# Kernel optimization log

Hardware: AMD Instinct MI355X
Metric: run time of the kernel (lower is better)

Reference implementation:

```python
import jax, jax.numpy as jnp
import numpy as np

N_NODES = 50000
N_EDGES = 800000
HID = 128
EDGE_DIM = 4
LAYERS = 4
MAX_Z = 100
NUM_GRAPHS = 512


def setup_inputs() -> dict:
    key = jax.random.key(0)
    ks = jax.random.split(key, 16)
    s = lambda k, shape, fan_in: jax.random.normal(k, shape, jnp.float32) / np.sqrt(fan_in)
    inp = {
        "z": jax.random.randint(ks[0], (N_NODES,), 0, MAX_Z + 1),
        "edge_index": jax.random.randint(ks[1], (2, N_EDGES), 0, N_NODES),
        "edge_attr": jax.random.normal(ks[2], (N_EDGES, EDGE_DIM), jnp.float32),
        "batch": jnp.sort(jax.random.randint(ks[3], (N_NODES,), 0, NUM_GRAPHS)),
        "emb": jax.random.normal(ks[4], (MAX_Z + 1, HID), jnp.float32),
        # stacked per-layer params; Linear stored as [in, out]
        "ew1": s(ks[5], (LAYERS, 2 * HID + EDGE_DIM, HID), 2 * HID + EDGE_DIM),
        "eb1": jnp.zeros((LAYERS, HID), jnp.float32),
        "ew2": s(ks[6], (LAYERS, HID, HID), HID),
        "eb2": jnp.zeros((LAYERS, HID), jnp.float32),
        "nw": s(ks[7], (LAYERS, 2 * HID, HID), 2 * HID),
        "nb": jnp.zeros((LAYERS, HID), jnp.float32),
        "rw1": s(ks[8], (HID, HID), HID),
        "rb1": jnp.zeros((HID,), jnp.float32),
        "rw2": s(ks[9], (HID, 1), HID),
        "rb2": jnp.zeros((1,), jnp.float32),
    }
    return inp


def _forward(z, edge_index, edge_attr, batch,
             emb, ew1, eb1, ew2, eb2, nw, nb, rw1, rb1, rw2, rb2):
    silu = jax.nn.silu
    src, dst = edge_index[0], edge_index[1]
    x = emb[z]  # [N, H]
    for l in range(LAYERS):
        m_in = jnp.concatenate([x[src], x[dst], edge_attr], axis=-1)  # [E, 2H+ed]
        h = silu(m_in @ ew1[l] + eb1[l])
        msg = silu(h @ ew2[l] + eb2[l])  # [E, H]
        agg = jax.ops.segment_sum(msg, dst, num_segments=N_NODES)  # scatter-add
        x = silu(jnp.concatenate([x, agg], axis=-1) @ nw[l] + nb[l])
    # segment mean over graphs
    sums = jax.ops.segment_sum(x, batch, num_segments=NUM_GRAPHS)
    counts = jnp.clip(jax.ops.segment_sum(jnp.ones((x.shape[0],), x.dtype), batch,
                                          num_segments=NUM_GRAPHS), 1.0)[:, None]
    g = sums / counts  # [G, H]
    pred = (silu(g @ rw1 + rb1) @ rw2 + rb2)[:, 0]  # [G]
    return pred


def reference(z, edge_index, edge_attr, batch,
              emb, ew1, eb1, ew2, eb2, nw, nb, rw1, rb1, rw2, rb2):
    return _forward(z, edge_index, edge_attr, batch,
                    emb, ew1, eb1, ew2, eb2, nw, nb, rw1, rb1, rw2, rb2)
```

## Files before the change

kernel.cpp:

```cpp
#include <hip/hip_runtime.h>
#include <hip/hip_bf16.h>
#include <math.h>

#define HID  128
#define EDIM 4

typedef unsigned short u16;
typedef u16    us8   __attribute__((ext_vector_type(8)));
typedef __bf16 bf16x8 __attribute__((ext_vector_type(8)));
typedef float  f32x4 __attribute__((ext_vector_type(4)));

__device__ __forceinline__ float silu_f(float v) {
    return v * __builtin_amdgcn_rcpf(1.0f + __expf(-v));
}
__device__ __forceinline__ u16 f2bf(float f) {
    unsigned u = __float_as_uint(f);
    unsigned r = u + 0x7fffu + ((u >> 16) & 1u);
    return (u16)(r >> 16);
}
__device__ __forceinline__ u16 f2bf_fast(float f) {
    return (u16)((__float_as_uint(f) + 0x8000u) >> 16);
}
__device__ __forceinline__ unsigned pack_bf2(float a, float b) {
    return ((__float_as_uint(a) + 0x8000u) >> 16) |
           ((__float_as_uint(b) + 0x8000u) & 0xffff0000u);
}
__device__ __forceinline__ float bf2f(u16 s) {
    return __uint_as_float(((unsigned)s) << 16);
}
__device__ __forceinline__ bf16x8 as_bf(us8 v) {
    return __builtin_bit_cast(bf16x8, v);
}
__device__ __forceinline__ f32x4 bf4f(ushort4 v) {
    f32x4 r;
    r[0] = bf2f(v.x); r[1] = bf2f(v.y); r[2] = bf2f(v.z); r[3] = bf2f(v.w);
    return r;
}

__device__ __forceinline__ void wfrag_gen(const float* __restrict__ w,
        u16* __restrict__ out, int KT, int Kdata, int Kstride,
        int split, int jump, int idx) {
    int lane = idx & 63;
    int f    = (idx >> 6) % (KT * 8);
    int l    = idx / (64 * KT * 8);
    int kt = f >> 3, nt = f & 7;
    int n  = nt * 16 + (lane & 15);
    int k0 = kt * 32 + ((lane >> 4) * 8);
    us8 v;
    #pragma unroll
    for (int j = 0; j < 8; ++j) {
        int k = k0 + j;
        int row = k + (k >= split ? jump : 0);
        v[j] = (row < Kdata) ? f2bf(w[((size_t)l * Kstride + row) * HID + n]) : (u16)0;
    }
    *(us8*)&out[((size_t)(l * KT * 8 + f) * 64 + lane) * 8] = v;
}

#define T1S (4 * 4 * 8 * 64)
#define T1T (4 * 1 * 8 * 64)
#define T1B (4 * 4 * 8 * 64)
#define T2  (4 * 4 * 8 * 64)
#define T3  (4 * 8 * 8 * 64)

__global__ __launch_bounds__(256) void setup_kernel(
        const float* __restrict__ ew1, const float* __restrict__ ew2,
        const float* __restrict__ nw,
        u16* __restrict__ w1sf, u16* __restrict__ w1tf,
        u16* __restrict__ w1bf,
        u16* __restrict__ w2f, u16* __restrict__ nwf,
        int* __restrict__ cnt, int* __restrict__ cursor,
        float* __restrict__ sums, float* __restrict__ cnts_g, int N, int G) {
    const int BIG = 1 << 30;
    int idx = blockIdx.x * 256 + threadIdx.x;
    if (idx < T1S) { wfrag_gen(ew1, w1sf, 4, 128, 260, BIG, 0, idx); return; }
    idx -= T1S;
    if (idx < T1T) { wfrag_gen(ew1, w1tf, 1, 260, 260, 0, 256, idx); return; }
    idx -= T1T;
    if (idx < T1B) { wfrag_gen(ew1, w1bf, 4, 260, 260, 0, 128, idx); return; }
    idx -= T1B;
    if (idx < T2) { wfrag_gen(ew2, w2f, 4, 128, 128, BIG, 0, idx); return; }
    idx -= T2;
    if (idx < T3) { wfrag_gen(nw, nwf, 8, 256, 256, BIG, 0, idx); return; }
    idx -= T3;
    if (idx < N) { cnt[idx] = 0; return; }
    idx -= N;
    if (idx < N) { cursor[idx] = 0; return; }
    idx -= N;
    if (idx < G * HID) { sums[idx] = 0.f; return; }
    idx -= G * HID;
    if (idx < G) { cnts_g[idx] = 0.f; return; }
}

__global__ __launch_bounds__(256) void hist_kernel(const int* __restrict__ dst,
        int* __restrict__ cnt, int E) {
    int e = blockIdx.x * 256 + threadIdx.x;
    if (e < E) atomicAdd(&cnt[dst[e]], 1);
}

__global__ __launch_bounds__(1024) void scan_kernel(const int* __restrict__ cnt,
        int* __restrict__ rowptr, int n) {
    __shared__ int s[1024];
    const int t = threadIdx.x;
    const int chunk = (n + 1023) >> 10;
    int lo = t * chunk, hi = lo + chunk;
    if (lo > n) lo = n;
    if (hi > n) hi = n;
    int sum = 0;
    for (int i = lo; i < hi; ++i) sum += cnt[i];
    s[t] = sum;
    __syncthreads();
    for (int off = 1; off < 1024; off <<= 1) {
        int v = (t >= off) ? s[t - off] : 0;
        __syncthreads();
        s[t] += v;
        __syncthreads();
    }
    int run = s[t] - sum;
    for (int i = lo; i < hi; ++i) { rowptr[i] = run; run += cnt[i]; }
    if (t == 1023) rowptr[n] = run;
}

__device__ __forceinline__ void dual_proj(
        const u16* __restrict__ xb,
        const u16* __restrict__ w1sf, const u16* __restrict__ w1bf,
        const float* __restrict__ b1n,
        u16* __restrict__ Ys, u16* __restrict__ Y,
        int i0, int n, int t) {
    const int wv   = t >> 6, lane = t & 63;
    const int lrow = lane & 15;
    const int kq   = lane >> 4;
    const int kq8  = kq * 8;

    int iN[2];
    #pragma unroll
    for (int mt = 0; mt < 2; ++mt) {
        int i = i0 + mt * 16 + lrow; if (i >= n) i = n - 1;
        iN[mt] = i;
    }
    f32x4 aS[2][2], aB[2][2];
    #pragma unroll
    for (int mt = 0; mt < 2; ++mt)
        #pragma unroll
        for (int nt = 0; nt < 2; ++nt) {
            aS[mt][nt] = (f32x4){0.f, 0.f, 0.f, 0.f};
            aB[mt][nt] = *(const f32x4*)&b1n[(wv * 2 + nt) * 16 + kq * 4];
        }

    #pragma unroll
    for (int kt = 0; kt < 4; ++kt) {
        bf16x8 ws0 = *(const bf16x8*)&w1sf[((size_t)(kt * 8 + wv * 2 + 0) * 64 + lane) * 8];
        bf16x8 ws1 = *(const bf16x8*)&w1sf[((size_t)(kt * 8 + wv * 2 + 1) * 64 + lane) * 8];
        bf16x8 wb0 = *(const bf16x8*)&w1bf[((size_t)(kt * 8 + wv * 2 + 0) * 64 + lane) * 8];
        bf16x8 wb1 = *(const bf16x8*)&w1bf[((size_t)(kt * 8 + wv * 2 + 1) * 64 + lane) * 8];
        #pragma unroll
        for (int mt = 0; mt < 2; ++mt) {
            bf16x8 a = as_bf(*(const us8*)&xb[(size_t)iN[mt] * HID + kt * 32 + kq8]);
            aS[mt][0] = __builtin_amdgcn_mfma_f32_16x16x32_bf16(ws0, a, aS[mt][0], 0, 0, 0);
            aS[mt][1] = __builtin_amdgcn_mfma_f32_16x16x32_bf16(ws1, a, aS[mt][1], 0, 0, 0);
            aB[mt][0] = __builtin_amdgcn_mfma_f32_16x16x32_bf16(wb0, a, aB[mt][0], 0, 0, 0);
            aB[mt][1] = __builtin_amdgcn_mfma_f32_16x16x32_bf16(wb1, a, aB[mt][1], 0, 0, 0);
        }
    }
    #pragma unroll
    for (int mt = 0; mt < 2; ++mt) {
        int node = i0 + mt * 16 + lrow;
        if (node < n) {
            #pragma unroll
            for (int nt = 0; nt < 2; ++nt) {
                uint2 sv, bv;
                sv.x = pack_bf2(aS[mt][nt][0], aS[mt][nt][1]);
                sv.y = pack_bf2(aS[mt][nt][2], aS[mt][nt][3]);
                bv.x = pack_bf2(aB[mt][nt][0], aB[mt][nt][1]);
                bv.y = pack_bf2(aB[mt][nt][2], aB[mt][nt][3]);
                *(uint2*)&Ys[(size_t)node * HID + (wv * 2 + nt) * 16 + kq * 4] = sv;
                *(uint2*)&Y [(size_t)node * HID + (wv * 2 + nt) * 16 + kq * 4] = bv;
            }
        }
    }
}

__global__ __launch_bounds__(256) void scatter_embed_kernel(
        const int* __restrict__ src, const int* __restrict__ dst,
        const float* __restrict__ ea, const int* __restrict__ rowptr,
        int* __restrict__ cursor, int4* __restrict__ es,
        const int* __restrict__ z, const float* __restrict__ emb,
        u16* __restrict__ xb, u16* __restrict__ agg,
        const int* __restrict__ batch, float* __restrict__ counts,
        const u16* __restrict__ w1sf, const u16* __restrict__ w1bf,
        const float* __restrict__ b1n,
        u16* __restrict__ Ys, u16* __restrict__ Y,
        int E, int n, int SB) {
    const int t = threadIdx.x;
    if ((int)blockIdx.x < SB) {
        int e = blockIdx.x * 256 + t;
        if (e >= E) return;
        int d = dst[e];
        int p = rowptr[d] + atomicAdd(&cursor[d], 1);
        const float* q = &ea[(size_t)e * EDIM];
        int4 rec;
        rec.x = src[e];
        rec.y = d;
        rec.z = (int)((unsigned)f2bf(q[0]) | ((unsigned)f2bf(q[1]) << 16));
        rec.w = (int)((unsigned)f2bf(q[2]) | ((unsigned)f2bf(q[3]) << 16));
        es[p] = rec;
    } else {
        const int i0 = (blockIdx.x - SB) * 32;
        #pragma unroll
        for (int j = 0; j < 16; ++j) {
            int idx = j * 256 + t;
            int node = i0 + (idx >> 7), col = idx & 127;
            if (node < n) {
                xb[(size_t)node * HID + col] = f2bf(emb[(size_t)z[node] * HID + col]);
                agg[(size_t)node * HID + col] = 0;
            }
        }
        if (t < 32 && i0 + t < n)
            unsafeAtomicAdd(&counts[batch[i0 + t]], 1.0f);
        __syncthreads();
        dual_proj(xb, w1sf, w1bf, b1n, Ys, Y, i0, n, t);
    }
}

__global__ __launch_bounds__(512, 8) void edge_mfma(
        const int4* __restrict__ es,
        const u16* __restrict__ w1tf,
        const u16* __restrict__ w2f, const float* __restrict__ b2,
        const u16* __restrict__ Ys, const u16* __restrict__ Y,
        u16* __restrict__ agg, int nE) {
    __shared__ __align__(16) char smem[64 * 132 * 4];
    __shared__ __align__(16) int dsh[64];
    __shared__ __align__(16) int ssh[64];
    u16*   A = (u16*)smem;
    u16*   H = (u16*)smem;
    float* M = (float*)smem;

    const int t    = threadIdx.x;
    const int e0   = blockIdx.x * 64;
    const int wv   = t >> 6, lane = t & 63;
    const int lrow = lane & 15;
    const int kq   = lane >> 4;
    const int kq8  = kq * 8;
    const int rq   = kq * 4;
    const int h    = wv >> 2;
    const int p    = wv & 3;

    if (t < 64) {
        int e = e0 + t;
        bool valid = e < nE; if (!valid) e = nE - 1;
        int4 rec = es[e];
        dsh[t] = valid ? rec.y : -1;
        ssh[t] = rec.x;
        int base = t * 40;
        us8 z8 = (us8){0, 0, 0, 0, 0, 0, 0, 0};
        *(us8*)&A[base + 8]  = z8;
        *(us8*)&A[base + 16] = z8;
        *(us8*)&A[base + 24] = z8;
        A[base + 0] = (u16)((unsigned)rec.z & 0xffffu);
        A[base + 1] = (u16)((unsigned)rec.z >> 16);
        A[base + 2] = (u16)((unsigned)rec.w & 0xffffu);
        A[base + 3] = (u16)((unsigned)rec.w >> 16);
        A[base + 4] = 0;   A[base + 5] = 0;   A[base + 6] = 0;   A[base + 7] = 0;
    }
    __syncthreads();

    f32x4 acc[2][2];
    #pragma unroll
    for (int mt = 0; mt < 2; ++mt) {
        int edge = (h * 2 + mt) * 16 + lrow;
        int d = dsh[edge]; if (d < 0) d = 0;
        int s = ssh[edge];
        #pragma unroll
        for (int nt = 0; nt < 2; ++nt) {
            ushort4 yv = *(const ushort4*)&Y [(size_t)d * HID + (p * 2 + nt) * 16 + rq];
            ushort4 sv = *(const ushort4*)&Ys[(size_t)s * HID + (p * 2 + nt) * 16 + rq];
            acc[mt][nt] = bf4f(yv) + bf4f(sv);
        }
    }
    {
        bf16x8 w0 = *(const bf16x8*)&w1tf[((size_t)(p * 2 + 0) * 64 + lane) * 8];
        bf16x8 w1 = *(const bf16x8*)&w1tf[((size_t)(p * 2 + 1) * 64 + lane) * 8];
        #pragma unroll
        for (int mt = 0; mt < 2; ++mt) {
            bf16x8 a = *(const bf16x8*)&A[((h * 2 + mt) * 16 + lrow) * 40 + kq8];
            acc[mt][0] = __builtin_amdgcn_mfma_f32_16x16x32_bf16(w0, a, acc[mt][0], 0, 0, 0);
            acc[mt][1] = __builtin_amdgcn_mfma_f32_16x16x32_bf16(w1, a, acc[mt][1], 0, 0, 0);
        }
    }
    __syncthreads();

    #pragma unroll
    for (int mt = 0; mt < 2; ++mt)
        #pragma unroll
        for (int nt = 0; nt < 2; ++nt) {
            uint2 hv;
            hv.x = pack_bf2(silu_f(acc[mt][nt][0]), silu_f(acc[mt][nt][1]));
            hv.y = pack_bf2(silu_f(acc[mt][nt][2]), silu_f(acc[mt][nt][3]));
            int edge = (h * 2 + mt) * 16 + lrow;
            *(uint2*)&H[edge * 136 + (p * 2 + nt) * 16 + rq] = hv;
        }
    __syncthreads();

    f32x4 acc2[2][2];
    #pragma unroll
    for (int nt = 0; nt < 2; ++nt) {
        f32x4 bv = *(const f32x4*)&b2[(p * 2 + nt) * 16 + rq];
        acc2[0][nt] = bv; acc2[1][nt] = bv;
    }
    #pragma unroll
    for (int kt = 0; kt < 4; ++kt) {
        bf16x8 w0 = *(const bf16x8*)&w2f[((size_t)(kt * 8 + p * 2 + 0) * 64 + lane) * 8];
        bf16x8 w1 = *(const bf16x8*)&w2f[((size_t)(kt * 8 + p * 2 + 1) * 64 + lane) * 8];
        #pragma unroll
        for (int mt = 0; mt < 2; ++mt) {
            bf16x8 a = *(const bf16x8*)&H[((h * 2 + mt) * 16 + lrow) * 136 + kt * 32 + kq8];
            acc2[mt][0] = __builtin_amdgcn_mfma_f32_16x16x32_bf16(w0, a, acc2[mt][0], 0, 0, 0);
            acc2[mt][1] = __builtin_amdgcn_mfma_f32_16x16x32_bf16(w1, a, acc2[mt][1], 0, 0, 0);
        }
    }
    __syncthreads();

    #pragma unroll
    for (int mt = 0; mt < 2; ++mt)
        #pragma unroll
        for (int nt = 0; nt < 2; ++nt) {
            f32x4 mv;
            #pragma unroll
            for (int r = 0; r < 4; ++r) mv[r] = silu_f(acc2[mt][nt][r]);
            int edge = (h * 2 + mt) * 16 + lrow;
            *(f32x4*)&M[edge * 132 + (p * 2 + nt) * 16 + rq] = mv;
        }

    {
        int col = p * 32 + (lane & 31);
        int r0  = h * 32 + (lane >> 5) * 16;
        int4 da = *(const int4*)&dsh[r0];
        int4 db = *(const int4*)&dsh[r0 + 4];
        int4 dc = *(const int4*)&dsh[r0 + 8];
        int4 dd = *(const int4*)&dsh[r0 + 12];
        int ds_[16] = {da.x, da.y, da.z, da.w, db.x, db.y, db.z, db.w,
                       dc.x, dc.y, dc.z, dc.w, dd.x, dd.y, dd.z, dd.w};
        float run = 0.f;
        int   cur = ds_[0];
        #pragma unroll
        for (int i = 0; i < 16; ++i) {
            run += M[(r0 + i) * 132 + col];
            int nxt = (i == 15) ? -2 : ds_[i + 1];
            if (cur != nxt) {
                float nbr = __shfl_xor(run, 1);
                if (cur >= 0 && !(col & 1)) {
                    __hip_bfloat162 v;
                    v.x = __float2bfloat16(run);
                    v.y = __float2bfloat16(nbr);
                    unsafeAtomicAdd(
                        (__hip_bfloat162*)&agg[(size_t)cur * HID + col], v);
                }
                run = 0.f; cur = nxt;
            }
        }
    }
}

__global__ __launch_bounds__(256) void node_mfma(
        u16* __restrict__ xb, u16* __restrict__ agg,
        const u16* __restrict__ nwf, const float* __restrict__ nb,
        const int* __restrict__ batch, float* __restrict__ sums,
        const u16* __restrict__ w1sf_nxt, const u16* __restrict__ w1bf_nxt,
        const float* __restrict__ b1_nxt,
        u16* __restrict__ Ys, u16* __restrict__ Y,
        int last, int n) {
    const int t    = threadIdx.x;
    const int i0   = blockIdx.x * 32;
    const int wv   = t >> 6, lane = t & 63;
    const int lrow = lane & 15;
    const int kq   = lane >> 4;
    const int kq8  = kq * 8;
    const int rq   = kq * 4;

    int iN[2];
    #pragma unroll
    for (int mt = 0; mt < 2; ++mt) {
        int i = i0 + mt * 16 + lrow; if (i >= n) i = n - 1;
        iN[mt] = i;
    }

    f32x4 acc[2][2];
    {
        float bias0 = nb[wv * 32 + lrow], bias1 = nb[wv * 32 + 16 + lrow];
        #pragma unroll
        for (int mt = 0; mt < 2; ++mt)
            #pragma unroll
            for (int r = 0; r < 4; ++r) {
                acc[mt][0][r] = bias0; acc[mt][1][r] = bias1;
            }
    }
    #pragma unroll
    for (int kt = 0; kt < 4; ++kt) {
        bf16x8 w0 = *(const bf16x8*)&nwf[((size_t)(kt * 8 + wv * 2 + 0) * 64 + lane) * 8];
        bf16x8 w1 = *(const bf16x8*)&nwf[((size_t)(kt * 8 + wv * 2 + 1) * 64 + lane) * 8];
        #pragma unroll
        for (int mt = 0; mt < 2; ++mt) {
            bf16x8 a = as_bf(*(const us8*)&xb[(size_t)iN[mt] * HID + kt * 32 + kq8]);
            acc[mt][0] = __builtin_amdgcn_mfma_f32_16x16x32_bf16(a, w0, acc[mt][0], 0, 0, 0);
            acc[mt][1] = __builtin_amdgcn_mfma_f32_16x16x32_bf16(a, w1, acc[mt][1], 0, 0, 0);
        }
    }
    #pragma unroll
    for (int kt = 4; kt < 8; ++kt) {
        bf16x8 w0 = *(const bf16x8*)&nwf[((size_t)(kt * 8 + wv * 2 + 0) * 64 + lane) * 8];
        bf16x8 w1 = *(const bf16x8*)&nwf[((size_t)(kt * 8 + wv * 2 + 1) * 64 + lane) * 8];
        #pragma unroll
        for (int mt = 0; mt < 2; ++mt) {
            bf16x8 a = as_bf(*(const us8*)&agg[(size_t)iN[mt] * HID + (kt - 4) * 32 + kq8]);
            acc[mt][0] = __builtin_amdgcn_mfma_f32_16x16x32_bf16(a, w0, acc[mt][0], 0, 0, 0);
            acc[mt][1] = __builtin_amdgcn_mfma_f32_16x16x32_bf16(a, w1, acc[mt][1], 0, 0, 0);
        }
    }

    if (!last) {
        __syncthreads();
        const us8 z8 = (us8){0, 0, 0, 0, 0, 0, 0, 0};
        #pragma unroll
        for (int kt = 0; kt < 4; ++kt)
            #pragma unroll
            for (int mt = 0; mt < 2; ++mt)
                *(us8*)&agg[(size_t)iN[mt] * HID + kt * 32 + kq8] = z8;
        #pragma unroll
        for (int mt = 0; mt < 2; ++mt)
            #pragma unroll
            for (int nt2 = 0; nt2 < 2; ++nt2)
                #pragma unroll
                for (int r = 0; r < 4; ++r) {
                    int i = i0 + mt * 16 + rq + r;
                    if (i < n)
                        xb[(size_t)i * HID + wv * 32 + nt2 * 16 + lrow] =
                            f2bf_fast(silu_f(acc[mt][nt2][r]));
                }
        __syncthreads();
        dual_proj(xb, w1sf_nxt, w1bf_nxt, b1_nxt, Ys, Y, i0, n, t);
    } else {
        #pragma unroll
        for (int mt = 0; mt < 2; ++mt)
            #pragma unroll
            for (int nt2 = 0; nt2 < 2; ++nt2)
                #pragma unroll
                for (int r = 0; r < 4; ++r) {
                    int i = i0 + mt * 16 + rq + r;
                    if (i < n) {
                        int b = batch[i];
                        unsafeAtomicAdd(&sums[(size_t)b * HID + wv * 32 + nt2 * 16 + lrow],
                                        silu_f(acc[mt][nt2][r]));
                    }
                }
    }
}

__global__ __launch_bounds__(HID) void readout_kernel(
        const float* __restrict__ sums, const float* __restrict__ counts,
        const float* __restrict__ rw1, const float* __restrict__ rb1,
        const float* __restrict__ rw2, const float* __restrict__ rb2,
        float* __restrict__ pred) {
    __shared__ float gv[HID];
    __shared__ float hv[HID];
    const int g = blockIdx.x;
    const int t = threadIdx.x;
    float c = counts[g];
    if (c < 1.0f) c = 1.0f;
    gv[t] = sums[(size_t)g * HID + t] / c;
    __syncthreads();
    float acc = rb1[t];
    for (int k4 = 0; k4 < 32; ++k4) {
        float4 mv = *(const float4*)&gv[k4 * 4];
        #pragma unroll
        for (int j = 0; j < 4; ++j)
            acc += ((const float*)&mv)[j] * rw1[(size_t)(k4 * 4 + j) * HID + t];
    }
    hv[t] = silu_f(acc) * rw2[t];
    __syncthreads();
    for (int s = HID / 2; s > 0; s >>= 1) {
        if (t < s) hv[t] += hv[t + s];
        __syncthreads();
    }
    if (t == 0) pred[g] = hv[0] + rb2[0];
}

extern "C" void kernel_launch(void* const* d_in, const int* in_sizes, int n_in,
                              void* d_out, int out_size, void* d_ws, size_t ws_size,
                              hipStream_t stream) {
    const int*   z          = (const int*)d_in[0];
    const int*   edge_index = (const int*)d_in[1];
    const float* edge_attr  = (const float*)d_in[2];
    const int*   batch      = (const int*)d_in[3];
    const float* emb        = (const float*)d_in[4];
    const float* ew1        = (const float*)d_in[5];
    const float* eb1        = (const float*)d_in[6];
    const float* ew2        = (const float*)d_in[7];
    const float* eb2        = (const float*)d_in[8];
    const float* nw         = (const float*)d_in[9];
    const float* nb         = (const float*)d_in[10];
    const float* rw1        = (const float*)d_in[11];
    const float* rb1        = (const float*)d_in[12];
    const float* rw2        = (const float*)d_in[13];
    const float* rb2        = (const float*)d_in[14];
    float* pred = (float*)d_out;

    const int N = in_sizes[0];
    const int E = in_sizes[1] / 2;
    const int G = out_size;
    const int* srcI = edge_index;
    const int* dstI = edge_index + E;

    char* base = (char*)d_ws;
    size_t off = 0;
    auto carve = [&](size_t bytes) -> char* {
        char* p = base + off;
        off = (off + bytes + 255) & ~(size_t)255;
        return p;
    };
    u16*   agg    = (u16*)carve((size_t)N * HID * sizeof(u16));
    float* sums   = (float*)carve((size_t)G * HID * sizeof(float));
    float* cnts_g = (float*)carve((size_t)G * sizeof(float));
    u16*   xb     = (u16*)carve((size_t)N * HID * sizeof(u16));
    u16*   Y      = (u16*)carve((size_t)N * HID * sizeof(u16));
    u16*   Ys     = (u16*)carve((size_t)N * HID * sizeof(u16));
    int4*  es     = (int4*)carve((size_t)(E + 64) * sizeof(int4));
    int*   rowptr = (int*)carve((size_t)(N + 1) * sizeof(int));
    int*   cursor = (int*)carve((size_t)N * sizeof(int));
    int*   cnt    = (int*)carve((size_t)N * sizeof(int));
    u16*   w1sf   = (u16*)carve((size_t)4 * 32 * 512 * sizeof(u16));
    u16*   w1tf   = (u16*)carve((size_t)4 * 8 * 512 * sizeof(u16));
    u16*   w1bf   = (u16*)carve((size_t)4 * 32 * 512 * sizeof(u16));
    u16*   w2f    = (u16*)carve((size_t)4 * 32 * 512 * sizeof(u16));
    u16*   nwf    = (u16*)carve((size_t)4 * 64 * 512 * sizeof(u16));

    {
        long long total = (long long)T1S + T1T + T1B + T2 + T3
                        + 2LL * N + (long long)G * HID + G;
        int blocks = (int)((total + 255) / 256);
        setup_kernel<<<blocks, 256, 0, stream>>>(ew1, ew2, nw, w1sf, w1tf, w1bf,
                                                 w2f, nwf, cnt, cursor,
                                                 sums, cnts_g, N, G);
    }

    hist_kernel<<<(E + 255) / 256, 256, 0, stream>>>(dstI, cnt, E);
    scan_kernel<<<1, 1024, 0, stream>>>(cnt, rowptr, N);

    {
        const int SB = (E + 255) / 256;
        const int EB = (N + 31) / 32;
        scatter_embed_kernel<<<SB + EB, 256, 0, stream>>>(
            srcI, dstI, edge_attr, rowptr, cursor, es,
            z, emb, xb, agg, batch, cnts_g, w1sf, w1bf, eb1, Ys, Y, E, N, SB);
    }

    for (int l = 0; l < 4; ++l) {
        edge_mfma<<<(E + 63) / 64, 512, 0, stream>>>(
            es,
            w1tf + (size_t)l * 8 * 512,
            w2f + (size_t)l * 32 * 512, eb2 + (size_t)l * HID,
            Ys, Y, agg, E);
        int lnxt = (l + 1) & 3;
        node_mfma<<<(N + 31) / 32, 256, 0, stream>>>(
            xb, agg, nwf + (size_t)l * 64 * 512, nb + (size_t)l * HID,
            batch, sums,
            w1sf + (size_t)lnxt * 32 * 512, w1bf + (size_t)lnxt * 32 * 512,
            eb1 + (size_t)lnxt * HID,
            Ys, Y, (l == 3) ? 1 : 0, N);
    }

    readout_kernel<<<G, HID, 0, stream>>>(sums, cnts_g, rw1, rb1, rw2, rb2, pred);
}
```

Before: 993.3 us.

## Fold histogram into setup kernel, memset zeroing, and overlap edge gathers with staging

```diff
diff --git a/kernel.cpp b/kernel.cpp
--- a/kernel.cpp
+++ b/kernel.cpp
@@ -68,8 +68,7 @@
         u16* __restrict__ w1sf, u16* __restrict__ w1tf,
         u16* __restrict__ w1bf,
         u16* __restrict__ w2f, u16* __restrict__ nwf,
-        int* __restrict__ cnt, int* __restrict__ cursor,
-        float* __restrict__ sums, float* __restrict__ cnts_g, int N, int G) {
+        const int* __restrict__ dstI, int* __restrict__ cnt, int E) {
     const int BIG = 1 << 30;
     int idx = blockIdx.x * 256 + threadIdx.x;
     if (idx < T1S) { wfrag_gen(ew1, w1sf, 4, 128, 260, BIG, 0, idx); return; }
@@ -82,19 +81,7 @@
     idx -= T2;
     if (idx < T3) { wfrag_gen(nw, nwf, 8, 256, 256, BIG, 0, idx); return; }
     idx -= T3;
-    if (idx < N) { cnt[idx] = 0; return; }
-    idx -= N;
-    if (idx < N) { cursor[idx] = 0; return; }
-    idx -= N;
-    if (idx < G * HID) { sums[idx] = 0.f; return; }
-    idx -= G * HID;
-    if (idx < G) { cnts_g[idx] = 0.f; return; }
-}
-
-__global__ __launch_bounds__(256) void hist_kernel(const int* __restrict__ dst,
-        int* __restrict__ cnt, int E) {
-    int e = blockIdx.x * 256 + threadIdx.x;
-    if (e < E) atomicAdd(&cnt[dst[e]], 1);
+    if (idx < E) atomicAdd(&cnt[dstI[idx]], 1);
 }
 
 __global__ __launch_bounds__(1024) void scan_kernel(const int* __restrict__ cnt,
@@ -229,7 +216,6 @@
         u16* __restrict__ agg, int nE) {
     __shared__ __align__(16) char smem[64 * 132 * 4];
     __shared__ __align__(16) int dsh[64];
-    __shared__ __align__(16) int ssh[64];
     u16*   A = (u16*)smem;
     u16*   H = (u16*)smem;
     float* M = (float*)smem;
@@ -249,7 +235,6 @@
         bool valid = e < nE; if (!valid) e = nE - 1;
         int4 rec = es[e];
         dsh[t] = valid ? rec.y : -1;
-        ssh[t] = rec.x;
         int base = t * 40;
         us8 z8 = (us8){0, 0, 0, 0, 0, 0, 0, 0};
         *(us8*)&A[base + 8]  = z8;
@@ -261,21 +246,28 @@
         A[base + 3] = (u16)((unsigned)rec.w >> 16);
         A[base + 4] = 0;   A[base + 5] = 0;   A[base + 6] = 0;   A[base + 7] = 0;
     }
-    __syncthreads();
 
     f32x4 acc[2][2];
-    #pragma unroll
-    for (int mt = 0; mt < 2; ++mt) {
-        int edge = (h * 2 + mt) * 16 + lrow;
-        int d = dsh[edge]; if (d < 0) d = 0;
-        int s = ssh[edge];
+    {
+        int eA = e0 + (h * 2 + 0) * 16 + lrow; if (eA >= nE) eA = nE - 1;
+        int eB = e0 + (h * 2 + 1) * 16 + lrow; if (eB >= nE) eB = nE - 1;
+        int4 recA = es[eA];
+        int4 recB = es[eB];
+        int dA = recA.y, sA = recA.x;
+        int dB = recB.y, sB = recB.x;
         #pragma unroll
         for (int nt = 0; nt < 2; ++nt) {
-            ushort4 yv = *(const ushort4*)&Y [(size_t)d * HID + (p * 2 + nt) * 16 + rq];
-            ushort4 sv = *(const ushort4*)&Ys[(size_t)s * HID + (p * 2 + nt) * 16 + rq];
-            acc[mt][nt] = bf4f(yv) + bf4f(sv);
-        }
-    }
+            int c = (p * 2 + nt) * 16 + rq;
+            ushort4 yA = *(const ushort4*)&Y [(size_t)dA * HID + c];
+            ushort4 sA4 = *(const ushort4*)&Ys[(size_t)sA * HID + c];
+            ushort4 yB = *(const ushort4*)&Y [(size_t)dB * HID + c];
+            ushort4 sB4 = *(const ushort4*)&Ys[(size_t)sB * HID + c];
+            acc[0][nt] = bf4f(yA) + bf4f(sA4);
+            acc[1][nt] = bf4f(yB) + bf4f(sB4);
+        }
+    }
+    __syncthreads();
+
     {
         bf16x8 w0 = *(const bf16x8*)&w1tf[((size_t)(p * 2 + 0) * 64 + lane) * 8];
         bf16x8 w1 = *(const bf16x8*)&w1tf[((size_t)(p * 2 + 1) * 64 + lane) * 8];
@@ -532,16 +524,16 @@
     u16*   w2f    = (u16*)carve((size_t)4 * 32 * 512 * sizeof(u16));
     u16*   nwf    = (u16*)carve((size_t)4 * 64 * 512 * sizeof(u16));
 
+    hipMemsetAsync(cursor, 0, (size_t)((char*)(cnt + N) - (char*)cursor), stream);
+    hipMemsetAsync(sums, 0, (size_t)((char*)(cnts_g + G) - (char*)sums), stream);
+
     {
-        long long total = (long long)T1S + T1T + T1B + T2 + T3
-                        + 2LL * N + (long long)G * HID + G;
+        long long total = (long long)T1S + T1T + T1B + T2 + T3 + E;
         int blocks = (int)((total + 255) / 256);
         setup_kernel<<<blocks, 256, 0, stream>>>(ew1, ew2, nw, w1sf, w1tf, w1bf,
-                                                 w2f, nwf, cnt, cursor,
-                                                 sums, cnts_g, N, G);
-    }
-
-    hist_kernel<<<(E + 255) / 256, 256, 0, stream>>>(dstI, cnt, E);
+                                                 w2f, nwf, dstI, cnt, E);
+    }
+
     scan_kernel<<<1, 1024, 0, stream>>>(cnt, rowptr, N);
 
     {
```

New measurement: 984.3 us. About the same (-0.9%).
